# Kernel optimization log

Hardware: AMD Instinct MI355X
Metric: run time of the kernel (lower is better)

## Reference

```python
import jax, jax.numpy as jnp
import numpy as np

B, S, I, H, O = 2048, 128, 1, 512, 1
OUT_SEQ_LEN = 24


def setup_inputs() -> dict:
    key = jax.random.key(0)
    ks = jax.random.split(key, 12)
    s = 1.0 / np.sqrt(H)
    u = lambda k, shape: jax.random.uniform(k, shape, jnp.float32, -s, s)
    return {
        'x': jax.random.normal(ks[0], (B, S, I), jnp.float32),
        'enc_Wih': u(ks[1], (H, I)),
        'enc_Whh': u(ks[2], (H, H)),
        'enc_bih': u(ks[3], (H,)),
        'enc_bhh': u(ks[4], (H,)),
        'dec_Wih': u(ks[5], (H, I)),
        'dec_Whh': u(ks[6], (H, H)),
        'dec_bih': u(ks[7], (H,)),
        'dec_bhh': u(ks[8], (H,)),
        'fc_W': u(ks[9], (O, H)),
        'fc_b': u(ks[10], (O,)),
    }


def reference(x, enc_Wih, enc_Whh, enc_bih, enc_bhh,
              dec_Wih, dec_Whh, dec_bih, dec_bhh, fc_W, fc_b):
    batch = x.shape[0]
    h0 = jnp.zeros((batch, H), x.dtype)

    # Encoder: vanilla tanh RNN, h_t = tanh(x_t W_ih^T + b_ih + h_{t-1} W_hh^T + b_hh)
    def enc_step(h, xt):
        h2 = jnp.tanh(xt @ enc_Wih.T + enc_bih + h @ enc_Whh.T + enc_bhh)
        return h2, None

    hT, _ = jax.lax.scan(enc_step, h0, jnp.swapaxes(x, 0, 1))  # scan over S

    def dec_step(carry, _):
        h, inp = carry
        h2 = jnp.tanh(inp @ dec_Wih.T + dec_bih + h @ dec_Whh.T + dec_bhh)
        out = h2 @ fc_W.T + fc_b  # [B, O]
        return (h2, out), out

    dec_in0 = x[:, -1, :]  # [B, I]
    _, outs = jax.lax.scan(dec_step, (hT, dec_in0), None, length=OUT_SEQ_LEN)
    outputs = jnp.swapaxes(outs, 0, 1)  # [B, OUT_SEQ_LEN, O]
    return outputs[..., 0]  # squeeze(-1) since O == 1
```

## Files before the change

kernel.cpp:

```cpp
#include <hip/hip_runtime.h>
#include <math.h>

#define BATCH 2048
#define SEQ   128
#define HID   512
#define OUTT  24
#define RPB   16
#define NBLK  (BATCH/RPB)
#define TPB   1024
#define NTW   2
#define KTN   (HID/32)
#define LDSB_KT 3
#define STR_KT  (KTN - LDSB_KT)
#define LDSB_BASE 0
#define STR_BASE  LDSB_KT
#define ATILE 8192
#define PFD   4
#define PRIME 2

typedef _Float16 half8 __attribute__((ext_vector_type(8)));
typedef float   floatx4 __attribute__((ext_vector_type(4)));

__device__ __forceinline__ void mfma_hv(floatx4& c, half8 a, half8 b) {
    c = __builtin_amdgcn_mfma_f32_16x16x32_f16(a, b, c, 0, 0, 0);
}

__device__ __forceinline__ float ftanh(float x) {
    float e = __builtin_amdgcn_exp2f(x * 2.885390081777927f);
    float r = __builtin_amdgcn_rcpf(e + 1.0f);
    return fmaf(-2.0f, r, 1.0f);
}

__global__ __launch_bounds__(256) void pack_wfrag(const float* __restrict__ W,
                                                  _Float16* __restrict__ Bw)
{
    int id   = blockIdx.x * 256 + threadIdx.x;
    int lane = id & 63;
    int nt   = (id >> 6) & 31;
    int kt   = id >> 11;
    int n  = nt * 16 + (lane & 15);
    int k0 = kt * 32 + (lane >> 4) * 8;
    const float* src = W + (size_t)n * HID + k0;
    half8 v;
    #pragma unroll
    for (int j = 0; j < 8; j++) v[j] = (_Float16)src[j];
    *(half8*)&Bw[(size_t)id * 8] = v;
}

__global__ __launch_bounds__(TPB)
__attribute__((amdgpu_waves_per_eu(4, 4)))
void rnn_persist(
    const float* __restrict__ x,
    const _Float16* __restrict__ BwE,
    const _Float16* __restrict__ BwD,
    const float* __restrict__ encWih, const float* __restrict__ encBih,
    const float* __restrict__ encBhh,
    const float* __restrict__ decWih, const float* __restrict__ decBih,
    const float* __restrict__ decBhh,
    const float* __restrict__ fcW, const float* __restrict__ fcB,
    float* __restrict__ out)
{
    __shared__ _Float16 A[2][ATILE];
    __shared__ _Float16 BwL[LDSB_KT * 16384];
    __shared__ float    xs[RPB][SEQ];
    __shared__ float    dec_in_s[RPB];

    const int tid  = threadIdx.x;
    const int lane = tid & 63;
    const int wv   = tid >> 6;
    const int row0 = blockIdx.x * RPB;
    const int c    = lane & 15;
    const int q    = lane >> 4;
    const int mB   = q * 4;

    const float fcb0 = fcB[0];

    int   nIdx[NTW];
    int   moff[NTW][4];
    float wiR[NTW], bbR[NTW];
    #pragma unroll
    for (int i = 0; i < NTW; i++) {
        int n = (wv * NTW + i) * 16 + c;
        nIdx[i] = n;
        int G = (n >> 3) & 3;
        int base = (n >> 5) * 512 + G * 128 + (n & 7);
        #pragma unroll
        for (int r = 0; r < 4; r++)
            moff[i][r] = base + (((mB + r) ^ G) << 3);
        wiR[i] = encWih[n];
        bbR[i] = encBih[n] + encBhh[n];
    }
    int   aFC[HID / 64];
    float fcw[HID / 64];
    #pragma unroll
    for (int ii = 0; ii < HID / 64; ii++) {
        int k = ii * 64 + lane;
        int G = (k >> 3) & 3;
        aFC[ii] = (k >> 5) * 512 + G * 128 + (k & 7) + ((wv ^ G) << 3);
        fcw[ii] = fcW[k];
    }

    {
        const float4* xg = (const float4*)(x + (size_t)row0 * SEQ);
        if (tid < RPB * SEQ / 4) ((float4*)xs)[tid] = xg[tid];
    }

    for (int i = tid; i < ATILE / 2; i += TPB) ((int*)A[0])[i] = 0;

    {
        const float4* src = (const float4*)(BwE + (size_t)LDSB_BASE * 16384);
        float4* dst = (float4*)BwL;
        #pragma unroll
        for (int i = 0; i < LDSB_KT * 16384 / 8 / TPB; i++)
            dst[i * TPB + tid] = src[i * TPB + tid];
    }

    const int    ldsAoff = q * 128 + ((c ^ q) << 3);
    const size_t bbase   = (size_t)(wv * NTW) * 512 + (size_t)lane * 8;
    const int    bbL     = wv * NTW * 512 + lane * 8;

    half8 sb[STR_KT][NTW];
    #pragma unroll
    for (int p = 0; p < PRIME; p++)
        #pragma unroll
        for (int i = 0; i < NTW; i++)
            sb[p][i] = *(const half8*)&BwE[bbase + (size_t)(STR_BASE + p) * 16384 + i * 512];

    __syncthreads();

    int cur = 0;
    for (int t = 0; t < SEQ + OUTT; t++) {
        const bool enc = (t < SEQ);
        const _Float16* __restrict__ Bw = enc ? BwE : BwD;

        if (t == SEQ) {
            #pragma unroll
            for (int i = 0; i < NTW; i++) {
                wiR[i] = decWih[nIdx[i]];
                bbR[i] = decBih[nIdx[i]] + decBhh[nIdx[i]];
            }
            const float4* src = (const float4*)(BwD + (size_t)LDSB_BASE * 16384);
            float4* dst = (float4*)BwL;
            #pragma unroll
            for (int i = 0; i < LDSB_KT * 16384 / 8 / TPB; i++)
                dst[i * TPB + tid] = src[i * TPB + tid];
            __syncthreads();
        }

        floatx4 acc[NTW];
        #pragma unroll
        for (int i = 0; i < NTW; i++) acc[i] = (floatx4){0.f, 0.f, 0.f, 0.f};

        __builtin_amdgcn_s_setprio(1);

        #pragma unroll
        for (int p = PRIME; p < PFD; p++)
            #pragma unroll
            for (int i = 0; i < NTW; i++)
                sb[p][i] = *(const half8*)&Bw[bbase + (size_t)(STR_BASE + p) * 16384 + i * 512];

        #pragma unroll
        for (int kl = 0; kl < LDSB_KT; kl++) {
            half8 a = *(const half8*)&A[cur][(LDSB_BASE + kl) * 512 + ldsAoff];
            #pragma unroll
            for (int i = 0; i < NTW; i++) {
                half8 b = *(const half8*)&BwL[kl * 16384 + bbL + i * 512];
                mfma_hv(acc[i], a, b);
            }
        }

        #pragma unroll
        for (int s = 0; s < STR_KT; s++) {
            const int kt = STR_BASE + s;
            if (s + PFD < STR_KT) {
                #pragma unroll
                for (int i = 0; i < NTW; i++)
                    sb[s + PFD][i] = *(const half8*)&Bw[bbase + (size_t)(kt + PFD) * 16384 + i * 512];
            }
            half8 a = *(const half8*)&A[cur][kt * 512 + ldsAoff];
            #pragma unroll
            for (int i = 0; i < NTW; i++)
                mfma_hv(acc[i], a, sb[s][i]);
        }

        __builtin_amdgcn_s_setprio(0);

        const int nxt = cur ^ 1;

        {
            const _Float16* __restrict__ Bwn = (t + 1 < SEQ) ? BwE : BwD;
            #pragma unroll
            for (int p = 0; p < PRIME; p++)
                #pragma unroll
                for (int i = 0; i < NTW; i++)
                    sb[p][i] = *(const half8*)&Bwn[bbase + (size_t)(STR_BASE + p) * 16384 + i * 512];
        }

        float inp[4];
        if (enc) {
            #pragma unroll
            for (int r = 0; r < 4; r++) inp[r] = xs[mB + r][t];
        } else if (t == SEQ) {
            #pragma unroll
            for (int r = 0; r < 4; r++) inp[r] = xs[mB + r][SEQ - 1];
        } else {
            #pragma unroll
            for (int r = 0; r < 4; r++) inp[r] = dec_in_s[mB + r];
        }

        #pragma unroll
        for (int i = 0; i < NTW; i++) {
            #pragma unroll
            for (int r = 0; r < 4; r++) {
                float v = ftanh(acc[i][r] + inp[r] * wiR[i] + bbR[i]);
                A[nxt][moff[i][r]] = (_Float16)v;
            }
        }
        __syncthreads();

        if (!enc) {
            const _Float16* An = A[nxt];
            float sfc = 0.f;
            #pragma unroll
            for (int ii = 0; ii < HID / 64; ii++)
                sfc = fmaf((float)An[aFC[ii]], fcw[ii], sfc);
            #pragma unroll
            for (int off = 32; off > 0; off >>= 1)
                sfc += __shfl_down(sfc, off, 64);
            if (lane == 0) {
                float o = sfc + fcb0;
                dec_in_s[wv] = o;
                out[(size_t)(row0 + wv) * OUTT + (t - SEQ)] = o;
            }
            __syncthreads();
        }
        cur = nxt;
    }
}

extern "C" void kernel_launch(void* const* d_in, const int* in_sizes, int n_in,
                              void* d_out, int out_size, void* d_ws, size_t ws_size,
                              hipStream_t stream)
{
    const float* x        = (const float*)d_in[0];
    const float* enc_Wih  = (const float*)d_in[1];
    const float* enc_Whh  = (const float*)d_in[2];
    const float* enc_bih  = (const float*)d_in[3];
    const float* enc_bhh  = (const float*)d_in[4];
    const float* dec_Wih  = (const float*)d_in[5];
    const float* dec_Whh  = (const float*)d_in[6];
    const float* dec_bih  = (const float*)d_in[7];
    const float* dec_bhh  = (const float*)d_in[8];
    const float* fc_W     = (const float*)d_in[9];
    const float* fc_b     = (const float*)d_in[10];
    float* out = (float*)d_out;

    const size_t wfrag = (size_t)HID * HID;
    _Float16* BwE = (_Float16*)d_ws;
    _Float16* BwD = BwE + wfrag;

    pack_wfrag<<<HID * HID / (256 * 8), 256, 0, stream>>>(enc_Whh, BwE);
    pack_wfrag<<<HID * HID / (256 * 8), 256, 0, stream>>>(dec_Whh, BwD);

    rnn_persist<<<NBLK, TPB, 0, stream>>>(
        x, BwE, BwD,
        enc_Wih, enc_bih, enc_bhh,
        dec_Wih, dec_bih, dec_bhh,
        fc_W, fc_b, out);
}
```

Before: 596.6 us.

## Process two 16-row batch tiles per block to reuse streamed weight fragments

Each block now handles 32 batch rows, as two 16-row MFMA tiles that share every weight fragment loaded from global memory or LDS. The block count halves to 64, which cuts total Whh streaming traffic per timestep. To make room for the doubled hidden-state buffers, the LDS-resident weight tiles drop from 3 to 2 and the prefetch depth shrinks. The trade-off is more register pressure, fewer blocks on the chip (64 vs 128 CUs' worth), and more per-block serial work per step.

```diff
diff --git a/kernel.cpp b/kernel.cpp
--- a/kernel.cpp
+++ b/kernel.cpp
@@ -5,17 +5,17 @@
 #define SEQ   128
 #define HID   512
 #define OUTT  24
-#define RPB   16
+#define RPB   32
 #define NBLK  (BATCH/RPB)
 #define TPB   1024
 #define NTW   2
 #define KTN   (HID/32)
-#define LDSB_KT 3
+#define LDSB_KT 2
 #define STR_KT  (KTN - LDSB_KT)
 #define LDSB_BASE 0
 #define STR_BASE  LDSB_KT
 #define ATILE 8192
-#define PFD   4
+#define PFD   3
 #define PRIME 2
 
 typedef _Float16 half8 __attribute__((ext_vector_type(8)));
@@ -60,7 +60,7 @@
     const float* __restrict__ fcW, const float* __restrict__ fcB,
     float* __restrict__ out)
 {
-    __shared__ _Float16 A[2][ATILE];
+    __shared__ _Float16 A[2][2][ATILE];
     __shared__ _Float16 BwL[LDSB_KT * 16384];
     __shared__ float    xs[RPB][SEQ];
     __shared__ float    dec_in_s[RPB];
@@ -75,13 +75,11 @@
 
     const float fcb0 = fcB[0];
 
-    int   nIdx[NTW];
     int   moff[NTW][4];
     float wiR[NTW], bbR[NTW];
     #pragma unroll
     for (int i = 0; i < NTW; i++) {
         int n = (wv * NTW + i) * 16 + c;
-        nIdx[i] = n;
         int G = (n >> 3) & 3;
         int base = (n >> 5) * 512 + G * 128 + (n & 7);
         #pragma unroll
@@ -90,22 +88,13 @@
         wiR[i] = encWih[n];
         bbR[i] = encBih[n] + encBhh[n];
     }
-    int   aFC[HID / 64];
-    float fcw[HID / 64];
-    #pragma unroll
-    for (int ii = 0; ii < HID / 64; ii++) {
-        int k = ii * 64 + lane;
-        int G = (k >> 3) & 3;
-        aFC[ii] = (k >> 5) * 512 + G * 128 + (k & 7) + ((wv ^ G) << 3);
-        fcw[ii] = fcW[k];
-    }
 
     {
         const float4* xg = (const float4*)(x + (size_t)row0 * SEQ);
         if (tid < RPB * SEQ / 4) ((float4*)xs)[tid] = xg[tid];
     }
 
-    for (int i = tid; i < ATILE / 2; i += TPB) ((int*)A[0])[i] = 0;
+    for (int i = tid; i < 2 * ATILE / 2; i += TPB) ((int*)A[0])[i] = 0;
 
     {
         const float4* src = (const float4*)(BwE + (size_t)LDSB_BASE * 16384);
@@ -136,8 +125,9 @@
         if (t == SEQ) {
             #pragma unroll
             for (int i = 0; i < NTW; i++) {
-                wiR[i] = decWih[nIdx[i]];
-                bbR[i] = decBih[nIdx[i]] + decBhh[nIdx[i]];
+                int n = (wv * NTW + i) * 16 + c;
+                wiR[i] = decWih[n];
+                bbR[i] = decBih[n] + decBhh[n];
             }
             const float4* src = (const float4*)(BwD + (size_t)LDSB_BASE * 16384);
             float4* dst = (float4*)BwL;
@@ -147,9 +137,12 @@
             __syncthreads();
         }
 
-        floatx4 acc[NTW];
-        #pragma unroll
-        for (int i = 0; i < NTW; i++) acc[i] = (floatx4){0.f, 0.f, 0.f, 0.f};
+        floatx4 acc0[NTW], acc1[NTW];
+        #pragma unroll
+        for (int i = 0; i < NTW; i++) {
+            acc0[i] = (floatx4){0.f, 0.f, 0.f, 0.f};
+            acc1[i] = (floatx4){0.f, 0.f, 0.f, 0.f};
+        }
 
         __builtin_amdgcn_s_setprio(1);
 
@@ -161,11 +154,13 @@
 
         #pragma unroll
         for (int kl = 0; kl < LDSB_KT; kl++) {
-            half8 a = *(const half8*)&A[cur][(LDSB_BASE + kl) * 512 + ldsAoff];
+            half8 a0 = *(const half8*)&A[cur][0][(LDSB_BASE + kl) * 512 + ldsAoff];
+            half8 a1 = *(const half8*)&A[cur][1][(LDSB_BASE + kl) * 512 + ldsAoff];
             #pragma unroll
             for (int i = 0; i < NTW; i++) {
                 half8 b = *(const half8*)&BwL[kl * 16384 + bbL + i * 512];
-                mfma_hv(acc[i], a, b);
+                mfma_hv(acc0[i], a0, b);
+                mfma_hv(acc1[i], a1, b);
             }
         }
 
@@ -177,10 +172,13 @@
                 for (int i = 0; i < NTW; i++)
                     sb[s + PFD][i] = *(const half8*)&Bw[bbase + (size_t)(kt + PFD) * 16384 + i * 512];
             }
-            half8 a = *(const half8*)&A[cur][kt * 512 + ldsAoff];
-            #pragma unroll
-            for (int i = 0; i < NTW; i++)
-                mfma_hv(acc[i], a, sb[s][i]);
+            half8 a0 = *(const half8*)&A[cur][0][kt * 512 + ldsAoff];
+            half8 a1 = *(const half8*)&A[cur][1][kt * 512 + ldsAoff];
+            #pragma unroll
+            for (int i = 0; i < NTW; i++) {
+                mfma_hv(acc0[i], a0, sb[s][i]);
+                mfma_hv(acc1[i], a1, sb[s][i]);
+            }
         }
 
         __builtin_amdgcn_s_setprio(0);
@@ -196,41 +194,54 @@
                     sb[p][i] = *(const half8*)&Bwn[bbase + (size_t)(STR_BASE + p) * 16384 + i * 512];
         }
 
-        float inp[4];
+        float inp0[4], inp1[4];
         if (enc) {
             #pragma unroll
-            for (int r = 0; r < 4; r++) inp[r] = xs[mB + r][t];
+            for (int r = 0; r < 4; r++) { inp0[r] = xs[mB + r][t]; inp1[r] = xs[16 + mB + r][t]; }
         } else if (t == SEQ) {
             #pragma unroll
-            for (int r = 0; r < 4; r++) inp[r] = xs[mB + r][SEQ - 1];
+            for (int r = 0; r < 4; r++) { inp0[r] = xs[mB + r][SEQ - 1]; inp1[r] = xs[16 + mB + r][SEQ - 1]; }
         } else {
             #pragma unroll
-            for (int r = 0; r < 4; r++) inp[r] = dec_in_s[mB + r];
+            for (int r = 0; r < 4; r++) { inp0[r] = dec_in_s[mB + r]; inp1[r] = dec_in_s[16 + mB + r]; }
         }
 
         #pragma unroll
         for (int i = 0; i < NTW; i++) {
             #pragma unroll
             for (int r = 0; r < 4; r++) {
-                float v = ftanh(acc[i][r] + inp[r] * wiR[i] + bbR[i]);
-                A[nxt][moff[i][r]] = (_Float16)v;
+                float v0 = ftanh(acc0[i][r] + inp0[r] * wiR[i] + bbR[i]);
+                float v1 = ftanh(acc1[i][r] + inp1[r] * wiR[i] + bbR[i]);
+                A[nxt][0][moff[i][r]] = (_Float16)v0;
+                A[nxt][1][moff[i][r]] = (_Float16)v1;
             }
         }
         __syncthreads();
 
         if (!enc) {
-            const _Float16* An = A[nxt];
-            float sfc = 0.f;
-            #pragma unroll
-            for (int ii = 0; ii < HID / 64; ii++)
-                sfc = fmaf((float)An[aFC[ii]], fcw[ii], sfc);
-            #pragma unroll
-            for (int off = 32; off > 0; off >>= 1)
-                sfc += __shfl_down(sfc, off, 64);
+            const _Float16* An0 = A[nxt][0];
+            const _Float16* An1 = A[nxt][1];
+            float s0 = 0.f, s1 = 0.f;
+            #pragma unroll
+            for (int ii = 0; ii < HID / 64; ii++) {
+                int k = ii * 64 + lane;
+                int G = (k >> 3) & 3;
+                int a0 = (k >> 5) * 512 + G * 128 + (k & 7) + ((wv ^ G) << 3);
+                float w = fcW[k];
+                s0 = fmaf((float)An0[a0], w, s0);
+                s1 = fmaf((float)An1[a0], w, s1);
+            }
+            #pragma unroll
+            for (int off = 32; off > 0; off >>= 1) {
+                s0 += __shfl_down(s0, off, 64);
+                s1 += __shfl_down(s1, off, 64);
+            }
             if (lane == 0) {
-                float o = sfc + fcb0;
-                dec_in_s[wv] = o;
-                out[(size_t)(row0 + wv) * OUTT + (t - SEQ)] = o;
+                float o0 = s0 + fcb0, o1 = s1 + fcb0;
+                dec_in_s[wv]      = o0;
+                dec_in_s[wv + 16] = o1;
+                out[(size_t)(row0 + wv) * OUTT + (t - SEQ)]      = o0;
+                out[(size_t)(row0 + 16 + wv) * OUTT + (t - SEQ)] = o1;
             }
             __syncthreads();
         }
```

Result: slower. 741.2 us (+24.2%).
